# Performance work log

Measured on AMD Instinct MI355X. Metric: run time of the kernel, lower is better.

Reference implementation:

```python
import jax, jax.numpy as jnp
import numpy as np

N, D_IN, Z, K = 65536, 512, 128, 1024


def setup_inputs() -> dict:
    key = jax.random.key(0)
    k1, k2, k3 = jax.random.split(key, 3)
    x = jax.random.normal(k1, (N, D_IN), dtype=jnp.float32)
    # Dense(z_units) params (glorot-ish scale)
    W = jax.random.normal(k2, (D_IN, Z), dtype=jnp.float32) * (1.0 / np.sqrt(D_IN))
    b = jnp.zeros((Z,), dtype=jnp.float32)
    # VQ codebook [k_discrete, z_units]
    codebook = jax.random.normal(k3, (K, Z), dtype=jnp.float32)
    return {"x": x, "W": W, "b": b, "codebook": codebook}


def reference(x, W, b, codebook):
    # z_embed: Dense projection to z_units
    z_continuous = x @ W + b  # [N, Z]
    # Euclidean distances to codebook entries, computed via the expanded
    # quadratic form (avoids materializing the [N, K, Z] broadcast tensor).
    sq = (jnp.sum(z_continuous * z_continuous, axis=-1, keepdims=True)
          - 2.0 * (z_continuous @ codebook.T)
          + jnp.sum(codebook * codebook, axis=-1))  # [N, K]
    distances = jnp.sqrt(jnp.maximum(sq, 0.0))
    k_nearest = jnp.argmin(distances, axis=-1)  # [N] int
    z_quantised = codebook[k_nearest]  # gather -> [N, Z]
    z_one_hot = jax.nn.one_hot(k_nearest, K, dtype=z_continuous.dtype)  # [N, K]
    # straight-through estimator
    z_straight_through = z_continuous + jax.lax.stop_gradient(z_quantised - z_continuous)
    # perplexity stats (stored as a layer attribute in the original; computed here
    # for faithfulness but not returned, matching call()'s return signature)
    avg_probs = jnp.mean(z_one_hot, axis=0)
    _perplexity = jnp.exp(-jnp.sum(avg_probs * jnp.log(avg_probs + 1e-10)))
    return (z_straight_through, z_quantised, z_continuous, z_one_hot)
```

## Files before the change

### kernel.cpp

```cpp
#include <hip/hip_runtime.h>
#include <cstddef>

#define NROWS 65536
#define DIN   512
#define ZDIM  128
#define KCB   1024

typedef float  f32x4  __attribute__((ext_vector_type(4)));
typedef short  short8 __attribute__((ext_vector_type(8)));
typedef __bf16 bf16x8 __attribute__((ext_vector_type(8)));
typedef unsigned short ushort_t;
typedef unsigned int   uint_t;
typedef unsigned long long u64_t;

#define CB_CHB 24576
#define CB_SPB 8192
#define W_CHB  24576
#define W_SPB  8192
#define CNORM_OFF 786432
#define WF_OFF    790528
#define WS_NEEDED (790528 + 393216)

__device__ inline ushort_t bf_rtn(float v) {
  uint_t u = __float_as_uint(v);
  uint_t r = (u + 0x7fffu + ((u >> 16) & 1u)) >> 16;
  return (ushort_t)r;
}
__device__ inline float bf_up(ushort_t b) { return __uint_as_float(((uint_t)b) << 16); }
__device__ inline bf16x8 as_bf(short8 s) {
  union { short8 s; bf16x8 b; } u; u.s = s; return u.b;
}
__device__ inline void split3(float v, ushort_t& s1, ushort_t& s2, ushort_t& s3) {
  s1 = bf_rtn(v);  float f1 = bf_up(s1);
  float r1 = v - f1; s2 = bf_rtn(r1); float f2 = bf_up(s2);
  float r2 = r1 - f2; s3 = bf_rtn(r2);
}

__device__ inline void refine_one(uint_t packed, int bm, int w,
    const float* __restrict__ zc, const float* __restrict__ cbk,
    const float* __restrict__ cnorm, u64_t* rowkey)
{
  const int col = packed & 1023;
  const int rowloc = (packed >> 10) & 31;
  const int r = w * 32 + rowloc;
  const float* zr = zc + ((size_t)bm * 128 + r) * ZDIM;
  const float* cr = cbk + (size_t)col * ZDIM;
  f32x4 dps = {0.f, 0.f, 0.f, 0.f}, aps = {0.f, 0.f, 0.f, 0.f};
#pragma unroll
  for (int u = 0; u < 32; ++u) {
    f32x4 zv = *(const f32x4*)(zr + u * 4);
    f32x4 cv = *(const f32x4*)(cr + u * 4);
    dps += zv * cv;
    aps += zv * zv;
  }
  float dot = (dps[0] + dps[1]) + (dps[2] + dps[3]);
  float A   = (aps[0] + aps[1]) + (aps[2] + aps[3]);
  float d = (A - 2.f * dot) + cnorm[col];
  uint_t db = __float_as_uint(d);
  db = (db & 0x80000000u) ? ~db : (db | 0x80000000u);
  u64_t key = ((u64_t)db << 32) | (uint_t)col;
  u64_t old = rowkey[r];
  while (key < old) {
    u64_t assumed = old;
    old = atomicCAS(&rowkey[r], assumed, key);
    if (old == assumed) break;
  }
}

__global__ __launch_bounds__(128) void ksplit2(
    const float* __restrict__ cbk, char* __restrict__ wsb)
{
  const int n = blockIdx.x, k = threadIdx.x;
  float v = cbk[(size_t)n * ZDIM + k];
  ushort_t s1, s2, s3; split3(v, s1, s2, s3);

  const int chunk = n >> 5, ct = (n >> 4) & 1;
  const int km = k & 31, ks = k >> 5;
  const int g = (km >> 2) & 3, h = (km >> 4) & 1, j = (km & 3) + 4 * h;
  const int l = 16 * g + (n & 15);
  char* base = wsb + chunk * CB_CHB + ct * 4096 + ks * 1024 + l * 16 + j * 2;
  *(ushort_t*)(base + 0 * CB_SPB) = s1;
  *(ushort_t*)(base + 1 * CB_SPB) = s2;
  *(ushort_t*)(base + 2 * CB_SPB) = s3;

  float c2 = v * v;
#pragma unroll
  for (int m = 1; m < 64; m <<= 1) c2 += __shfl_xor(c2, m);
  __shared__ float wsum[2];
  if ((threadIdx.x & 63) == 0) wsum[threadIdx.x >> 6] = c2;
  __syncthreads();
  if (threadIdx.x == 0)
    *(float*)(wsb + CNORM_OFF + (size_t)n * 4) = wsum[0] + wsum[1];
}

__global__ __launch_bounds__(256) void wsplit(
    const float* __restrict__ W, char* __restrict__ wsb)
{
  const int idx = blockIdx.x * 256 + threadIdx.x;
  const int k = idx >> 7, col = idx & 127;
  float v = W[(size_t)k * ZDIM + col];
  ushort_t s1, s2, s3; split3(v, s1, s2, s3);

  const int kc = k >> 5, km = k & 31;
  const int g = (km >> 2) & 3, h = (km >> 4) & 1, j = (km & 3) + 4 * h;
  const int ct = col >> 4, l = 16 * g + (col & 15);
  char* base = wsb + WF_OFF + kc * W_CHB + ct * 1024 + l * 16 + j * 2;
  *(ushort_t*)(base + 0 * W_SPB) = s1;
  *(ushort_t*)(base + 1 * W_SPB) = s2;
  *(ushort_t*)(base + 2 * W_SPB) = s3;
}

__global__ __launch_bounds__(256, 2) void k1_oh(
    const float* __restrict__ x, const char* __restrict__ wfs,
    const float* __restrict__ b, float* __restrict__ z,
    float* __restrict__ oh)
{
  __shared__ __align__(16) char wbuf[2 * W_CHB];

  const int t = threadIdx.x, w = t >> 6, l = t & 63;
  const int g = l >> 4, c16 = l & 15;
  const int bm = blockIdx.x;

  f32x4 acc[2][8];
#pragma unroll
  for (int rt = 0; rt < 2; ++rt)
#pragma unroll
    for (int ct = 0; ct < 8; ++ct) acc[rt][ct] = (f32x4){0.f, 0.f, 0.f, 0.f};

  const size_t rowb[2] = {
    ((size_t)bm * 128 + w * 32 + 0 * 16 + c16) * DIN,
    ((size_t)bm * 128 + w * 32 + 1 * 16 + c16) * DIN };

  f32x4 wreg[6];
#pragma unroll
  for (int it = 0; it < 6; ++it)
    wreg[it] = *(const f32x4*)(wfs + it * 4096 + t * 16);
  f32x4 xcur[2][2];
#pragma unroll
  for (int rt = 0; rt < 2; ++rt)
#pragma unroll
    for (int h = 0; h < 2; ++h)
      xcur[rt][h] = *(const f32x4*)(x + rowb[rt] + 4 * g + 16 * h);
#pragma unroll
  for (int it = 0; it < 6; ++it)
    *(f32x4*)(wbuf + it * 4096 + t * 16) = wreg[it];
  __syncthreads();

  for (int kc = 0; kc < 16; ++kc) {
    const char* buf = wbuf + (size_t)(kc & 1) * W_CHB;
    const bool more = (kc + 1) < 16;
    f32x4 xnext[2][2];
    if (more) {
#pragma unroll
      for (int it = 0; it < 6; ++it)
        wreg[it] = *(const f32x4*)(wfs + (size_t)(kc + 1) * W_CHB + it * 4096 + t * 16);
#pragma unroll
      for (int rt = 0; rt < 2; ++rt)
#pragma unroll
        for (int h = 0; h < 2; ++h)
          xnext[rt][h] = *(const f32x4*)(x + rowb[rt] + (kc + 1) * 32 + 4 * g + 16 * h);
    }

    {
      float* orow = oh + ((size_t)bm * 128 + kc * 8 + (t >> 5)) * KCB + (t & 31) * 4;
      const f32x4 zv4 = {0.f, 0.f, 0.f, 0.f};
#pragma unroll
      for (int u = 0; u < 8; ++u)
        __builtin_nontemporal_store(zv4, (f32x4*)(orow + u * 128));
    }

    short8 a1[2], a2[2], a3[2];
#pragma unroll
    for (int rt = 0; rt < 2; ++rt)
#pragma unroll
      for (int h = 0; h < 2; ++h)
#pragma unroll
        for (int j = 0; j < 4; ++j) {
          ushort_t q1, q2, q3; split3(xcur[rt][h][j], q1, q2, q3);
          a1[rt][4 * h + j] = (short)q1;
          a2[rt][4 * h + j] = (short)q2;
          a3[rt][4 * h + j] = (short)q3;
        }

#pragma unroll
    for (int ct = 0; ct < 8; ++ct) {
      const char* bp = buf + ct * 1024 + l * 16;
      short8 b1 = *(const short8*)(bp + 0 * W_SPB);
      short8 b2 = *(const short8*)(bp + 1 * W_SPB);
      short8 b3 = *(const short8*)(bp + 2 * W_SPB);
#pragma unroll
      for (int rt = 0; rt < 2; ++rt) {
        f32x4 a = acc[rt][ct];
        a = __builtin_amdgcn_mfma_f32_16x16x32_bf16(as_bf(a1[rt]), as_bf(b1), a, 0, 0, 0);
        a = __builtin_amdgcn_mfma_f32_16x16x32_bf16(as_bf(a1[rt]), as_bf(b2), a, 0, 0, 0);
        a = __builtin_amdgcn_mfma_f32_16x16x32_bf16(as_bf(a2[rt]), as_bf(b1), a, 0, 0, 0);
        a = __builtin_amdgcn_mfma_f32_16x16x32_bf16(as_bf(a1[rt]), as_bf(b3), a, 0, 0, 0);
        a = __builtin_amdgcn_mfma_f32_16x16x32_bf16(as_bf(a2[rt]), as_bf(b2), a, 0, 0, 0);
        a = __builtin_amdgcn_mfma_f32_16x16x32_bf16(as_bf(a3[rt]), as_bf(b1), a, 0, 0, 0);
        acc[rt][ct] = a;
      }
    }

    if (more) {
      char* nbuf = wbuf + (size_t)((kc + 1) & 1) * W_CHB;
#pragma unroll
      for (int it = 0; it < 6; ++it)
        *(f32x4*)(nbuf + it * 4096 + t * 16) = wreg[it];
#pragma unroll
      for (int rt = 0; rt < 2; ++rt)
#pragma unroll
        for (int h = 0; h < 2; ++h) xcur[rt][h] = xnext[rt][h];
    }
    __syncthreads();
  }

#pragma unroll
  for (int ct = 0; ct < 8; ++ct) {
    float bb = b[ct * 16 + c16];
#pragma unroll
    for (int rt = 0; rt < 2; ++rt)
#pragma unroll
      for (int i = 0; i < 4; ++i) {
        size_t row = (size_t)bm * 128 + w * 32 + rt * 16 + 4 * g + i;
        z[row * ZDIM + ct * 16 + c16] = acc[rt][ct][i] + bb;
      }
  }
}

__global__ __launch_bounds__(256, 2) void k2f(
    const float* __restrict__ zc, const float* __restrict__ cbk,
    const char* __restrict__ cbs, const float* __restrict__ cnorm,
    float* __restrict__ zst, float* __restrict__ zq, float* __restrict__ oh)
{
  __shared__ __align__(16) char sm[16384];
  __shared__ u64_t rowkey[128];
  __shared__ uint_t wpool[4][128];
  __shared__ int wcnt[4];
  __shared__ int karr[128];

  const int t = threadIdx.x, w = t >> 6, l = t & 63;
  const int g = l >> 4, c16 = l & 15;
  const int bm = blockIdx.x;

  if (t < 128) rowkey[t] = ~0ull;
  if (t < 4) wcnt[t] = 0;

  short8 a1f[2][4];
  float anorm[2][4];
#pragma unroll
  for (int rt = 0; rt < 2; ++rt) {
    const size_t rb = ((size_t)bm * 128 + w * 32 + rt * 16 + c16) * ZDIM;
    float psum = 0.f;
#pragma unroll
    for (int ks = 0; ks < 4; ++ks)
#pragma unroll
      for (int h = 0; h < 2; ++h) {
        f32x4 v = *(const f32x4*)(zc + rb + ks * 32 + 4 * g + 16 * h);
#pragma unroll
        for (int j = 0; j < 4; ++j) {
          a1f[rt][ks][4 * h + j] = (short)bf_rtn(v[j]);
          psum += v[j] * v[j];
        }
      }
    psum += __shfl_xor(psum, 16);
    psum += __shfl_xor(psum, 32);
#pragma unroll
    for (int i = 0; i < 4; ++i) anorm[rt][i] = __shfl(psum, 4 * g + i);
  }

  float m1[2][4];
#pragma unroll
  for (int rt = 0; rt < 2; ++rt)
#pragma unroll
    for (int i = 0; i < 4; ++i) m1[rt][i] = 3.402823466e38f;

  f32x4 streg[2];
#pragma unroll
  for (int it = 0; it < 2; ++it)
    streg[it] = *(const f32x4*)(cbs + it * 4096 + t * 16);
#pragma unroll
  for (int it = 0; it < 2; ++it)
    *(f32x4*)(sm + it * 4096 + t * 16) = streg[it];
  __syncthreads();

  for (int c = 0; c < 32; ++c) {
    const char* buf = sm + (size_t)(c & 1) * 8192;
    const bool more = (c + 1) < 32;
    if (more) {
#pragma unroll
      for (int it = 0; it < 2; ++it)
        streg[it] = *(const f32x4*)(cbs + (size_t)(c + 1) * CB_CHB + it * 4096 + t * 16);
    }
    const float cn0 = cnorm[c * 32 + c16];
    const float cn1 = cnorm[c * 32 + 16 + c16];

#pragma unroll
    for (int ct = 0; ct < 2; ++ct) {
      f32x4 pa[2];
#pragma unroll
      for (int rt = 0; rt < 2; ++rt) pa[rt] = (f32x4){0.f, 0.f, 0.f, 0.f};
#pragma unroll
      for (int ks = 0; ks < 4; ++ks) {
        short8 b1 = *(const short8*)(buf + ct * 4096 + ks * 1024 + l * 16);
#pragma unroll
        for (int rt = 0; rt < 2; ++rt)
          pa[rt] = __builtin_amdgcn_mfma_f32_16x16x32_bf16(as_bf(a1f[rt][ks]), as_bf(b1), pa[rt], 0, 0, 0);
      }
      const float cn = ct ? cn1 : cn0;
#pragma unroll
      for (int rt = 0; rt < 2; ++rt)
#pragma unroll
        for (int i = 0; i < 4; ++i) {
          float f = (anorm[rt][i] - 2.f * pa[rt][i]) + cn;
          m1[rt][i] = fminf(m1[rt][i], f);
        }
    }

    if (more) {
      char* nbuf = sm + (size_t)((c + 1) & 1) * 8192;
#pragma unroll
      for (int it = 0; it < 2; ++it)
        *(f32x4*)(nbuf + it * 4096 + t * 16) = streg[it];
    }
    __syncthreads();
  }

#pragma unroll
  for (int m = 1; m < 16; m <<= 1)
#pragma unroll
    for (int rt = 0; rt < 2; ++rt)
#pragma unroll
      for (int i = 0; i < 4; ++i)
        m1[rt][i] = fminf(m1[rt][i], __shfl_xor(m1[rt][i], m));

  float thr[2][4];
#pragma unroll
  for (int rt = 0; rt < 2; ++rt)
#pragma unroll
    for (int i = 0; i < 4; ++i)
      thr[rt][i] = m1[rt][i] + 0.25f * sqrtf(anorm[rt][i]);

#pragma unroll
  for (int it = 0; it < 2; ++it)
    streg[it] = *(const f32x4*)(cbs + it * 4096 + t * 16);
#pragma unroll
  for (int it = 0; it < 2; ++it)
    *(f32x4*)(sm + it * 4096 + t * 16) = streg[it];
  __syncthreads();

  for (int c = 0; c < 32; ++c) {
    const char* buf = sm + (size_t)(c & 1) * 8192;
    const bool more = (c + 1) < 32;
    if (more) {
#pragma unroll
      for (int it = 0; it < 2; ++it)
        streg[it] = *(const f32x4*)(cbs + (size_t)(c + 1) * CB_CHB + it * 4096 + t * 16);
    }
    const float cn0 = cnorm[c * 32 + c16];
    const float cn1 = cnorm[c * 32 + 16 + c16];

#pragma unroll
    for (int ct = 0; ct < 2; ++ct) {
      f32x4 pa[2];
#pragma unroll
      for (int rt = 0; rt < 2; ++rt) pa[rt] = (f32x4){0.f, 0.f, 0.f, 0.f};
#pragma unroll
      for (int ks = 0; ks < 4; ++ks) {
        short8 b1 = *(const short8*)(buf + ct * 4096 + ks * 1024 + l * 16);
#pragma unroll
        for (int rt = 0; rt < 2; ++rt)
          pa[rt] = __builtin_amdgcn_mfma_f32_16x16x32_bf16(as_bf(a1f[rt][ks]), as_bf(b1), pa[rt], 0, 0, 0);
      }
      const float cn = ct ? cn1 : cn0;
      const int colb = c * 32 + ct * 16 + c16;
#pragma unroll
      for (int rt = 0; rt < 2; ++rt)
#pragma unroll
        for (int i = 0; i < 4; ++i) {
          float f = (anorm[rt][i] - 2.f * pa[rt][i]) + cn;
          if (f <= thr[rt][i]) {
            uint_t packed = (uint_t)colb | ((uint_t)(rt * 16 + 4 * g + i) << 10);
            int slot = atomicAdd(&wcnt[w], 1);
            if (slot < 128) wpool[w][slot] = packed;
            else refine_one(packed, bm, w, zc, cbk, cnorm, rowkey);
          }
        }
    }

    if (more) {
      char* nbuf = sm + (size_t)((c + 1) & 1) * 8192;
#pragma unroll
      for (int it = 0; it < 2; ++it)
        *(f32x4*)(nbuf + it * 4096 + t * 16) = streg[it];
    }
    __syncthreads();
  }

  int cnt = wcnt[w]; if (cnt > 128) cnt = 128;
  for (int s = l; s < cnt; s += 64)
    refine_one(wpool[w][s], bm, w, zc, cbk, cnorm, rowkey);
  __syncthreads();
  if (t < 128) karr[t] = (int)(rowkey[t] & 1023ull);
  __syncthreads();

#pragma unroll
  for (int it = 0; it < 16; ++it) {
    const int idx = it * 256 + t;
    const int r = idx >> 5, cq = (idx & 31) * 4;
    f32x4 v = *(const f32x4*)&cbk[(size_t)karr[r] * ZDIM + cq];
    const size_t off = ((size_t)bm * 128 + r) * ZDIM + cq;
    __builtin_nontemporal_store(v, (f32x4*)(zst + off));
    __builtin_nontemporal_store(v, (f32x4*)(zq + off));
  }

  if (t < 128) {
    oh[(size_t)(bm * 128 + t) * KCB + karr[t]] = 1.0f;
  }
}

__global__ __launch_bounds__(256) void k1_gemm(
    const float* __restrict__ x, const float* __restrict__ W,
    const float* __restrict__ b, float* __restrict__ z)
{
  __shared__ float xs[32][68];
  __shared__ float ws[32][132];

  const int t  = threadIdx.x;
  const int tx = t & 15, ty = t >> 4;
  const int bm = blockIdx.x;

  float acc[4][8];
#pragma unroll
  for (int i = 0; i < 4; ++i)
#pragma unroll
    for (int j = 0; j < 8; ++j) acc[i][j] = 0.f;

  const int sr  = t >> 2;
  const int skb = (t & 3) * 8;
  const int wkk = t >> 3;
  const int wcol = (t & 7) * 16;

  for (int k0 = 0; k0 < DIN; k0 += 32) {
    float4 v0 = *reinterpret_cast<const float4*>(&x[(size_t)(bm * 64 + sr) * DIN + k0 + skb]);
    float4 v1 = *reinterpret_cast<const float4*>(&x[(size_t)(bm * 64 + sr) * DIN + k0 + skb + 4]);
    xs[skb + 0][sr] = v0.x; xs[skb + 1][sr] = v0.y; xs[skb + 2][sr] = v0.z; xs[skb + 3][sr] = v0.w;
    xs[skb + 4][sr] = v1.x; xs[skb + 5][sr] = v1.y; xs[skb + 6][sr] = v1.z; xs[skb + 7][sr] = v1.w;
#pragma unroll
    for (int u = 0; u < 4; ++u) {
      float4 wv = *reinterpret_cast<const float4*>(&W[(size_t)(k0 + wkk) * ZDIM + wcol + u * 4]);
      *reinterpret_cast<float4*>(&ws[wkk][wcol + u * 4]) = wv;
    }
    __syncthreads();
#pragma unroll
    for (int kk = 0; kk < 32; ++kk) {
      float4 xv = *reinterpret_cast<float4*>(&xs[kk][ty * 4]);
      float4 wa = *reinterpret_cast<float4*>(&ws[kk][tx * 4]);
      float4 wb = *reinterpret_cast<float4*>(&ws[kk][64 + tx * 4]);
      float xr[4] = {xv.x, xv.y, xv.z, xv.w};
      float wr[8] = {wa.x, wa.y, wa.z, wa.w, wb.x, wb.y, wb.z, wb.w};
#pragma unroll
      for (int i = 0; i < 4; ++i)
#pragma unroll
        for (int j = 0; j < 8; ++j) acc[i][j] += xr[i] * wr[j];
    }
    __syncthreads();
  }

  float4 ba = *reinterpret_cast<const float4*>(&b[tx * 4]);
  float4 bb = *reinterpret_cast<const float4*>(&b[64 + tx * 4]);
#pragma unroll
  for (int i = 0; i < 4; ++i) {
    size_t row = (size_t)bm * 64 + ty * 4 + i;
    float4 oa = {acc[i][0] + ba.x, acc[i][1] + ba.y, acc[i][2] + ba.z, acc[i][3] + ba.w};
    float4 ob = {acc[i][4] + bb.x, acc[i][5] + bb.y, acc[i][6] + bb.z, acc[i][7] + bb.w};
    *reinterpret_cast<float4*>(&z[row * ZDIM + tx * 4]) = oa;
    *reinterpret_cast<float4*>(&z[row * ZDIM + 64 + tx * 4]) = ob;
  }
}

__global__ __launch_bounds__(256) void k2_vq(
    const float* __restrict__ zc, const float* __restrict__ cbk,
    float* __restrict__ zst, float* __restrict__ zq, float* __restrict__ oh)
{
  __shared__ float zt[128][68];
  __shared__ float ct[32][132];
  __shared__ float pc[128][2];
  __shared__ float csqc[128];
  __shared__ float Ap[64][4];
  __shared__ float Al[64];
  __shared__ float fbuf[64][17];
  __shared__ int   ibuf[64][17];
  __shared__ int   karr[64];

  const int t  = threadIdx.x;
  const int tx = t & 15, ty = t >> 4;
  const int bm = blockIdx.x;

  {
    const int r = t >> 2, kb = (t & 3) * 32;
    float asum = 0.f;
#pragma unroll
    for (int u = 0; u < 8; ++u) {
      float4 v = *reinterpret_cast<const float4*>(&zc[(size_t)(bm * 64 + r) * ZDIM + kb + u * 4]);
      zt[kb + u * 4 + 0][r] = v.x; zt[kb + u * 4 + 1][r] = v.y;
      zt[kb + u * 4 + 2][r] = v.z; zt[kb + u * 4 + 3][r] = v.w;
      asum += v.x * v.x + v.y * v.y + v.z * v.z + v.w * v.w;
    }
    Ap[r][t & 3] = asum;
  }
  __syncthreads();
  if (t < 64) Al[t] = (Ap[t][0] + Ap[t][1]) + (Ap[t][2] + Ap[t][3]);

  float fmin[4];
  int   kmin[4];
#pragma unroll
  for (int i = 0; i < 4; ++i) { fmin[i] = 3.4e38f; kmin[i] = 0; }

  const int scol = t >> 1, skb = (t & 1) * 16;

  for (int chunk = 0; chunk < 8; ++chunk) {
    float acc[4][8];
#pragma unroll
    for (int i = 0; i < 4; ++i)
#pragma unroll
      for (int j = 0; j < 8; ++j) acc[i][j] = 0.f;
    float cpart = 0.f;

    for (int ks = 0; ks < 4; ++ks) {
      __syncthreads();
#pragma unroll
      for (int u = 0; u < 4; ++u) {
        float4 v = *reinterpret_cast<const float4*>(
            &cbk[(size_t)(chunk * 128 + scol) * ZDIM + ks * 32 + skb + u * 4]);
        ct[skb + u * 4 + 0][scol] = v.x; ct[skb + u * 4 + 1][scol] = v.y;
        ct[skb + u * 4 + 2][scol] = v.z; ct[skb + u * 4 + 3][scol] = v.w;
        cpart += v.x * v.x + v.y * v.y + v.z * v.z + v.w * v.w;
      }
      __syncthreads();
#pragma unroll
      for (int kk = 0; kk < 32; ++kk) {
        float4 xv = *reinterpret_cast<float4*>(&zt[ks * 32 + kk][ty * 4]);
        float4 wa = *reinterpret_cast<float4*>(&ct[kk][tx * 4]);
        float4 wb = *reinterpret_cast<float4*>(&ct[kk][64 + tx * 4]);
        float xr[4] = {xv.x, xv.y, xv.z, xv.w};
        float wr[8] = {wa.x, wa.y, wa.z, wa.w, wb.x, wb.y, wb.z, wb.w};
#pragma unroll
        for (int i = 0; i < 4; ++i)
#pragma unroll
          for (int j = 0; j < 8; ++j) acc[i][j] += xr[i] * wr[j];
      }
    }

    pc[scol][t & 1] = cpart;
    __syncthreads();
    if (t < 128) csqc[t] = pc[t][0] + pc[t][1];
    __syncthreads();

#pragma unroll
    for (int i = 0; i < 4; ++i) {
      float Ar = Al[ty * 4 + i];
#pragma unroll
      for (int j = 0; j < 8; ++j) {
        int colL = (j < 4) ? (tx * 4 + j) : (64 + tx * 4 + (j - 4));
        float B = 2.f * acc[i][j];
        float f = (Ar - B) + csqc[colL];
        int col = chunk * 128 + colL;
        if (f < fmin[i] || (f == fmin[i] && col < kmin[i])) { fmin[i] = f; kmin[i] = col; }
      }
    }
  }

#pragma unroll
  for (int i = 0; i < 4; ++i) { fbuf[ty * 4 + i][tx] = fmin[i]; ibuf[ty * 4 + i][tx] = kmin[i]; }
  __syncthreads();
  if (t < 64) {
    float bf = fbuf[t][0]; int bi = ibuf[t][0];
    for (int e = 1; e < 16; ++e) {
      float f2 = fbuf[t][e]; int i2 = ibuf[t][e];
      if (f2 < bf || (f2 == bf && i2 < bi)) { bf = f2; bi = i2; }
    }
    karr[t] = bi;
  }
  __syncthreads();

  for (int it = 0; it < 32; ++it) {
    int r = it * 2 + (t >> 7);
    int col = t & 127;
    size_t row = (size_t)bm * 64 + r;
    float v = cbk[(size_t)karr[r] * ZDIM + col];
    zst[row * ZDIM + col] = v;
    zq[row * ZDIM + col] = v;
  }

  for (int r = 0; r < 64; ++r) {
    int k = karr[r];
    float4 v = {0.f, 0.f, 0.f, 0.f};
    if ((k >> 2) == t) {
      float* vv = reinterpret_cast<float*>(&v);
      vv[k & 3] = 1.f;
    }
    *reinterpret_cast<float4*>(&oh[(size_t)(bm * 64 + r) * KCB + t * 4]) = v;
  }
}

extern "C" void kernel_launch(void* const* d_in, const int* in_sizes, int n_in,
                              void* d_out, int out_size, void* d_ws, size_t ws_size,
                              hipStream_t stream) {
  const float* x   = (const float*)d_in[0];
  const float* W   = (const float*)d_in[1];
  const float* b   = (const float*)d_in[2];
  const float* cbk = (const float*)d_in[3];

  float* out = (float*)d_out;
  float* zst = out;
  float* zq  = out + (size_t)NROWS * ZDIM;
  float* zc  = out + (size_t)2 * NROWS * ZDIM;
  float* oh  = out + (size_t)3 * NROWS * ZDIM;

  if (ws_size >= (size_t)WS_NEEDED) {
    char* wsb = (char*)d_ws;
    ksplit2<<<KCB, 128, 0, stream>>>(cbk, wsb);
    wsplit<<<256, 256, 0, stream>>>(W, wsb);
    k1_oh<<<NROWS / 128, 256, 0, stream>>>(x, wsb + WF_OFF, b, zc, oh);
    k2f<<<NROWS / 128, 256, 0, stream>>>(
        zc, cbk, wsb, (const float*)(wsb + CNORM_OFF), zst, zq, oh);
  } else {
    k1_gemm<<<NROWS / 64, 256, 0, stream>>>(x, W, b, zc);
    k2_vq<<<NROWS / 64, 256, 0, stream>>>(zc, cbk, zst, zq, oh);
  }
}
```

Measured before the change: 150.5 us.

## Fuse VQ distance passes into single pass with running-min threshold; split one-hot zeroing

The distance kernel now runs the codebook MFMA sweep once instead of twice. After each chunk it reduces the running minimum across lanes and collects candidates against that running threshold, rather than against a final threshold found in a separate first pass. Because the running minimum is looser early on, more candidates reach the refine stage, so the per-wave candidate pool grows from 128 to 192 entries. Zeroing the one-hot output moves out of the projection GEMM loop into 256 extra dedicated blocks of the first kernel, which write large contiguous streams of zeros.

```diff
diff --git a/kernel.cpp b/kernel.cpp
--- a/kernel.cpp
+++ b/kernel.cpp
@@ -20,6 +20,8 @@
 #define CNORM_OFF 786432
 #define WF_OFF    790528
 #define WS_NEEDED (790528 + 393216)
+
+#define POOL_CAP 192
 
 __device__ inline ushort_t bf_rtn(float v) {
   uint_t u = __float_as_uint(v);
@@ -110,12 +112,22 @@
   *(ushort_t*)(base + 2 * W_SPB) = s3;
 }
 
-__global__ __launch_bounds__(256, 2) void k1_oh(
+__global__ __launch_bounds__(256, 2) void k1f(
     const float* __restrict__ x, const char* __restrict__ wfs,
     const float* __restrict__ b, float* __restrict__ z,
     float* __restrict__ oh)
 {
   __shared__ __align__(16) char wbuf[2 * W_CHB];
+
+  if (blockIdx.x >= 512) {
+    const size_t tid = (size_t)(blockIdx.x - 512) * 256 + threadIdx.x;
+    const f32x4 zv = {0.f, 0.f, 0.f, 0.f};
+    f32x4* dst = (f32x4*)oh + tid;
+#pragma unroll 8
+    for (int it = 0; it < 256; ++it)
+      __builtin_nontemporal_store(zv, dst + (size_t)it * 65536);
+    return;
+  }
 
   const int t = threadIdx.x, w = t >> 6, l = t & 63;
   const int g = l >> 4, c16 = l & 15;
@@ -159,14 +171,6 @@
 #pragma unroll
         for (int h = 0; h < 2; ++h)
           xnext[rt][h] = *(const f32x4*)(x + rowb[rt] + (kc + 1) * 32 + 4 * g + 16 * h);
-    }
-
-    {
-      float* orow = oh + ((size_t)bm * 128 + kc * 8 + (t >> 5)) * KCB + (t & 31) * 4;
-      const f32x4 zv4 = {0.f, 0.f, 0.f, 0.f};
-#pragma unroll
-      for (int u = 0; u < 8; ++u)
-        __builtin_nontemporal_store(zv4, (f32x4*)(orow + u * 128));
     }
 
     short8 a1[2], a2[2], a3[2];
@@ -227,14 +231,14 @@
   }
 }
 
-__global__ __launch_bounds__(256, 2) void k2f(
+__global__ __launch_bounds__(256, 2) void k2f1(
     const float* __restrict__ zc, const float* __restrict__ cbk,
     const char* __restrict__ cbs, const float* __restrict__ cnorm,
     float* __restrict__ zst, float* __restrict__ zq, float* __restrict__ oh)
 {
   __shared__ __align__(16) char sm[16384];
   __shared__ u64_t rowkey[128];
-  __shared__ uint_t wpool[4][128];
+  __shared__ uint_t wpool[4][POOL_CAP];
   __shared__ int wcnt[4];
   __shared__ int karr[128];
 
@@ -268,11 +272,15 @@
     for (int i = 0; i < 4; ++i) anorm[rt][i] = __shfl(psum, 4 * g + i);
   }
 
+  float thr_add[2][4];
   float m1[2][4];
 #pragma unroll
   for (int rt = 0; rt < 2; ++rt)
 #pragma unroll
-    for (int i = 0; i < 4; ++i) m1[rt][i] = 3.402823466e38f;
+    for (int i = 0; i < 4; ++i) {
+      thr_add[rt][i] = 0.25f * sqrtf(anorm[rt][i]);
+      m1[rt][i] = 3.402823466e38f;
+    }
 
   f32x4 streg[2];
 #pragma unroll
@@ -294,6 +302,7 @@
     const float cn0 = cnorm[c * 32 + c16];
     const float cn1 = cnorm[c * 32 + 16 + c16];
 
+    float fv[2][2][4];
 #pragma unroll
     for (int ct = 0; ct < 2; ++ct) {
       f32x4 pa[2];
@@ -312,76 +321,30 @@
 #pragma unroll
         for (int i = 0; i < 4; ++i) {
           float f = (anorm[rt][i] - 2.f * pa[rt][i]) + cn;
+          fv[ct][rt][i] = f;
           m1[rt][i] = fminf(m1[rt][i], f);
         }
     }
 
-    if (more) {
-      char* nbuf = sm + (size_t)((c + 1) & 1) * 8192;
-#pragma unroll
-      for (int it = 0; it < 2; ++it)
-        *(f32x4*)(nbuf + it * 4096 + t * 16) = streg[it];
-    }
-    __syncthreads();
-  }
-
-#pragma unroll
-  for (int m = 1; m < 16; m <<= 1)
-#pragma unroll
-    for (int rt = 0; rt < 2; ++rt)
-#pragma unroll
-      for (int i = 0; i < 4; ++i)
-        m1[rt][i] = fminf(m1[rt][i], __shfl_xor(m1[rt][i], m));
-
-  float thr[2][4];
-#pragma unroll
-  for (int rt = 0; rt < 2; ++rt)
-#pragma unroll
-    for (int i = 0; i < 4; ++i)
-      thr[rt][i] = m1[rt][i] + 0.25f * sqrtf(anorm[rt][i]);
-
-#pragma unroll
-  for (int it = 0; it < 2; ++it)
-    streg[it] = *(const f32x4*)(cbs + it * 4096 + t * 16);
-#pragma unroll
-  for (int it = 0; it < 2; ++it)
-    *(f32x4*)(sm + it * 4096 + t * 16) = streg[it];
-  __syncthreads();
-
-  for (int c = 0; c < 32; ++c) {
-    const char* buf = sm + (size_t)(c & 1) * 8192;
-    const bool more = (c + 1) < 32;
-    if (more) {
-#pragma unroll
-      for (int it = 0; it < 2; ++it)
-        streg[it] = *(const f32x4*)(cbs + (size_t)(c + 1) * CB_CHB + it * 4096 + t * 16);
-    }
-    const float cn0 = cnorm[c * 32 + c16];
-    const float cn1 = cnorm[c * 32 + 16 + c16];
+#pragma unroll
+    for (int m = 1; m < 16; m <<= 1)
+#pragma unroll
+      for (int rt = 0; rt < 2; ++rt)
+#pragma unroll
+        for (int i = 0; i < 4; ++i)
+          m1[rt][i] = fminf(m1[rt][i], __shfl_xor(m1[rt][i], m));
 
 #pragma unroll
     for (int ct = 0; ct < 2; ++ct) {
-      f32x4 pa[2];
-#pragma unroll
-      for (int rt = 0; rt < 2; ++rt) pa[rt] = (f32x4){0.f, 0.f, 0.f, 0.f};
-#pragma unroll
-      for (int ks = 0; ks < 4; ++ks) {
-        short8 b1 = *(const short8*)(buf + ct * 4096 + ks * 1024 + l * 16);
-#pragma unroll
-        for (int rt = 0; rt < 2; ++rt)
-          pa[rt] = __builtin_amdgcn_mfma_f32_16x16x32_bf16(as_bf(a1f[rt][ks]), as_bf(b1), pa[rt], 0, 0, 0);
-      }
-      const float cn = ct ? cn1 : cn0;
       const int colb = c * 32 + ct * 16 + c16;
 #pragma unroll
       for (int rt = 0; rt < 2; ++rt)
 #pragma unroll
         for (int i = 0; i < 4; ++i) {
-          float f = (anorm[rt][i] - 2.f * pa[rt][i]) + cn;
-          if (f <= thr[rt][i]) {
+          if (fv[ct][rt][i] <= m1[rt][i] + thr_add[rt][i]) {
             uint_t packed = (uint_t)colb | ((uint_t)(rt * 16 + 4 * g + i) << 10);
             int slot = atomicAdd(&wcnt[w], 1);
-            if (slot < 128) wpool[w][slot] = packed;
+            if (slot < POOL_CAP) wpool[w][slot] = packed;
             else refine_one(packed, bm, w, zc, cbk, cnorm, rowkey);
           }
         }
@@ -396,7 +359,7 @@
     __syncthreads();
   }
 
-  int cnt = wcnt[w]; if (cnt > 128) cnt = 128;
+  int cnt = wcnt[w]; if (cnt > POOL_CAP) cnt = POOL_CAP;
   for (int s = l; s < cnt; s += 64)
     refine_one(wpool[w][s], bm, w, zc, cbk, cnorm, rowkey);
   __syncthreads();
@@ -621,8 +584,8 @@
     char* wsb = (char*)d_ws;
     ksplit2<<<KCB, 128, 0, stream>>>(cbk, wsb);
     wsplit<<<256, 256, 0, stream>>>(W, wsb);
-    k1_oh<<<NROWS / 128, 256, 0, stream>>>(x, wsb + WF_OFF, b, zc, oh);
-    k2f<<<NROWS / 128, 256, 0, stream>>>(
+    k1f<<<768, 256, 0, stream>>>(x, wsb + WF_OFF, b, zc, oh);
+    k2f1<<<NROWS / 128, 256, 0, stream>>>(
         zc, cbk, wsb, (const float*)(wsb + CNORM_OFF), zst, zq, oh);
   } else {
     k1_gemm<<<NROWS / 64, 256, 0, stream>>>(x, W, b, zc);
```

Result: slower. 249.8 us (+66.0%).
